# Kernel optimization log

Measured on AMD Instinct MI355X. Metric: run time of the kernel, lower is better.

## Reference

```python
import jax, jax.numpy as jnp
import numpy as np

GAMMA = 1.0 - 2.0 ** (-5)   # 0.96875, as in the module
NUM_GROUPS = 8
NUM_HEADS = 8
EPS = 1e-5


def setup_inputs() -> dict:
    key = jax.random.key(0)
    ks = jax.random.split(key, 8)
    M, S, Hd = 128, 512, 512  # num_segments, bonds per segment, hidden_size
    N = M * S
    return {
        "message": jax.random.normal(ks[0], (N, Hd), jnp.float32),
        "Wq": jax.random.normal(ks[1], (Hd, Hd), jnp.float32) / np.sqrt(Hd).astype(np.float32),
        "Wk": jax.random.normal(ks[2], (Hd, Hd), jnp.float32) / np.sqrt(Hd).astype(np.float32),
        "Wv": jax.random.normal(ks[3], (Hd, Hd), jnp.float32) / np.sqrt(Hd).astype(np.float32),
        "Wo": jax.random.normal(ks[4], (Hd, Hd), jnp.float32) / np.sqrt(Hd).astype(np.float32),
        "bo": jax.random.normal(ks[5], (Hd,), jnp.float32) * 0.01,
        "gn_w": jnp.ones((Hd,), jnp.float32),
        "gn_b": jnp.zeros((Hd,), jnp.float32),
        "num_segs": M,
        "seg_len": S,
    }


def _forward(message, Wq, Wk, Wv, Wo, bo, gn_w, gn_b, M, S):
    Hd = message.shape[1]
    H = NUM_HEADS
    d = Hd // H
    scale = jnp.float32(d ** (-0.5))
    gamma = jnp.float32(GAMMA)

    x = message.reshape(M, S, Hd)                       # equal contiguous segments
    q = (x @ Wq.T).reshape(M, S, H, d)
    k = (x @ Wk.T).reshape(M, S, H, d)
    v = (x @ Wv.T).reshape(M, S, H, d)

    # per-segment K^T V outer-product state contribution: [M, H, d, d]
    A = jnp.einsum('mshd,mshe->mhde', k, v)
    decay = gamma ** S  # gamma ** b_size for equal segments

    def step(r, a):
        # r = K_i^T V_i + gamma^{b_size} * r_prev  (state AFTER segment i, as in source)
        r_new = a + decay * r
        return r_new, r_new

    _, r_all = jax.lax.scan(step, jnp.zeros((H, d, d), x.dtype), A)  # [M, H, d, d]

    # intra-segment retention: (Q K^T) * scale @ V
    scores = jnp.einsum('mshd,mthd->mhst', q, k) * scale
    intra = jnp.einsum('mhst,mthd->mshd', scores, v)
    # cross/recurrent term: (Q @ r_i) * gamma^{i+1}  (note: NOT scaled by scale_factor)
    cross = jnp.einsum('mshd,mhde->mshe', q, r_all)
    g = (gamma ** jnp.arange(1, M + 1, dtype=jnp.float32))[:, None, None, None]
    h = jax.nn.relu(intra + cross * g)                  # activation; dropout p=0

    out = h.reshape(M, S, Hd) @ Wo.T + bo               # W_b_o
    res = x + out                                       # residual (dropout p=0)

    # GroupNorm(8, hidden): per segment (batch N=1), groups over hidden channels,
    # stats pooled over (hidden/8 group channels x S bonds)
    gsh = res.reshape(M, S, NUM_GROUPS, Hd // NUM_GROUPS)
    mean = gsh.mean(axis=(1, 3), keepdims=True)
    var = gsh.var(axis=(1, 3), keepdims=True)
    normed = ((gsh - mean) * jax.lax.rsqrt(var + EPS)).reshape(M, S, Hd)
    normed = normed * gn_w + gn_b

    flat = normed.reshape(M * S, Hd)
    # cached_zero_vector is prepended once before the first segment
    return jnp.concatenate([jnp.zeros((1, Hd), flat.dtype), flat], axis=0)


def reference(message, Wq, Wk, Wv, Wo, bo, gn_w, gn_b, num_segs, seg_len):
    return _forward(message, Wq, Wk, Wv, Wo, bo, gn_w, gn_b, num_segs, seg_len)
```

## Files before the change

kernel.cpp:

```cpp
#include <hip/hip_runtime.h>
#include <math.h>

#define M_SEG 128
#define S_SEG 512
#define HD 512
#define NHEAD 8
#define DHEAD 64
#define NROWS (M_SEG * S_SEG)
#define QKVLD 1536
#define GAMMA_F 0.96875f
#define SCALE_F 0.125f

typedef unsigned short u16;
typedef float f32x4 __attribute__((ext_vector_type(4)));
typedef __bf16 bf16x8 __attribute__((ext_vector_type(8)));
typedef unsigned short ushort8 __attribute__((ext_vector_type(8)));
typedef unsigned short ushort4v __attribute__((ext_vector_type(4)));

__device__ __forceinline__ u16 f2bf(float f) {
    union { float f; unsigned u; } x; x.f = f;
    unsigned r = x.u + 0x7FFFu + ((x.u >> 16) & 1u);
    return (u16)(r >> 16);
}
__device__ __forceinline__ float bf2f(u16 v) {
    union { unsigned u; float f; } x; x.u = ((unsigned)v) << 16;
    return x.f;
}

__device__ __forceinline__ void gload16(const u16* g, u16* l) {
    __builtin_amdgcn_global_load_lds(
        (const __attribute__((address_space(1))) void*)g,
        (__attribute__((address_space(3))) void*)l, 16, 0, 0);
}

__global__ __launch_bounds__(256) void convert_bf16(const float* __restrict__ in,
                                                    u16* __restrict__ outp, int n8)
{
    int idx = blockIdx.x * 256 + threadIdx.x;
    if (idx >= n8) return;
    const float4 a = *reinterpret_cast<const float4*>(&in[(size_t)idx * 8]);
    const float4 b = *reinterpret_cast<const float4*>(&in[(size_t)idx * 8 + 4]);
    ushort8 o;
    o[0] = f2bf(a.x); o[1] = f2bf(a.y); o[2] = f2bf(a.z); o[3] = f2bf(a.w);
    o[4] = f2bf(b.x); o[5] = f2bf(b.y); o[6] = f2bf(b.z); o[7] = f2bf(b.w);
    *reinterpret_cast<ushort8*>(&outp[(size_t)idx * 8]) = o;
}

__global__ __launch_bounds__(256) void convert_weights(const float* __restrict__ w0,
                                                       const float* __restrict__ w1,
                                                       const float* __restrict__ w2,
                                                       const float* __restrict__ w3,
                                                       u16* __restrict__ outp)
{
    const int which = blockIdx.y;
    const float* src = which == 0 ? w0 : which == 1 ? w1 : which == 2 ? w2 : w3;
    u16* dst = outp + (size_t)which * 262144;
    int idx = blockIdx.x * 256 + threadIdx.x;
    const float4 a = *reinterpret_cast<const float4*>(&src[(size_t)idx * 8]);
    const float4 b = *reinterpret_cast<const float4*>(&src[(size_t)idx * 8 + 4]);
    ushort8 o;
    o[0] = f2bf(a.x); o[1] = f2bf(a.y); o[2] = f2bf(a.z); o[3] = f2bf(a.w);
    o[4] = f2bf(b.x); o[5] = f2bf(b.y); o[6] = f2bf(b.z); o[7] = f2bf(b.w);
    *reinterpret_cast<ushort8*>(&dst[(size_t)idx * 8]) = o;
}

template<int EPI>
__global__ __launch_bounds__(512, 1) void gemm8p(const u16* __restrict__ A, int lda,
                                                 const u16* __restrict__ B,
                                                 u16* __restrict__ Cv, int ldc, int ntile,
                                                 const u16* __restrict__ Xb,
                                                 const float* __restrict__ bias)
{
    __shared__ __align__(16) u16 sm[49152];
    const int t    = threadIdx.x;
    const int lane = t & 63;
    const int w    = t >> 6;
    const int wrow = w >> 2;
    const int wcol = w & 3;

    const int nwg  = gridDim.x;
    const int cpx  = nwg >> 3;
    const int bid  = blockIdx.x;
    const int sbid = (bid & 7) * cpx + (bid >> 3);
    const int mt = sbid / ntile, nt = sbid % ntile;
    const int rowBase = mt * 256, colBase = nt * 256;

    const int srow = t >> 2;
    const int sks  = (t & 3) ^ ((srow >> 1) & 3);
    const size_t gA0 = (size_t)(rowBase +       srow) * lda + sks * 8;
    const size_t gA1 = (size_t)(rowBase + 128 + srow) * lda + sks * 8;
    const size_t gB0 = (size_t)(colBase +       srow) * HD  + sks * 8;
    const size_t gB1 = (size_t)(colBase + 128 + srow) * HD  + sks * 8;

    f32x4 acc[8][4];
#pragma unroll
    for (int i = 0; i < 8; ++i)
#pragma unroll
        for (int j = 0; j < 4; ++j)
            acc[i][j] = (f32x4){0.f, 0.f, 0.f, 0.f};

#define STAGE_A(kt, buf)                                                     \
    do {                                                                     \
        gload16(&A[gA0 + (kt) * 32], &sm[(buf) * 16384 + t * 8]);            \
        gload16(&A[gA1 + (kt) * 32], &sm[(buf) * 16384 + 4096 + t * 8]);     \
    } while (0)
#define STAGE_B(kt, buf)                                                     \
    do {                                                                     \
        gload16(&B[gB0 + (kt) * 32], &sm[(buf) * 16384 + 8192 + t * 8]);     \
        gload16(&B[gB1 + (kt) * 32], &sm[(buf) * 16384 + 12288 + t * 8]);    \
    } while (0)

    STAGE_A(0, 0); STAGE_B(0, 0);
    STAGE_A(1, 1); STAGE_B(1, 1);

    const int frow = lane & 15;
    const int fkc  = lane >> 4;

#pragma unroll 1
    for (int kt = 0; kt < 16; ++kt) {
        const int buf = kt % 3;
        const int nbuf = (kt + 2) % 3;

        if (kt < 15) asm volatile("s_waitcnt vmcnt(4)" ::: "memory");
        else         asm volatile("s_waitcnt vmcnt(0)" ::: "memory");
        __builtin_amdgcn_s_barrier();
        __builtin_amdgcn_sched_barrier(0);

        if (kt < 14) STAGE_A(kt + 2, nbuf);
        const u16* Ab = &sm[buf * 16384];
        const u16* Bb = &sm[buf * 16384 + 8192];
        bf16x8 af[4], bfv[4];
#pragma unroll
        for (int mf = 0; mf < 4; ++mf) {
            const int r = wrow * 128 + mf * 16 + frow;
            af[mf] = *reinterpret_cast<const bf16x8*>(&Ab[r * 32 + ((fkc ^ ((r >> 1) & 3)) << 3)]);
        }
#pragma unroll
        for (int nn = 0; nn < 4; ++nn) {
            const int r = wcol * 64 + nn * 16 + frow;
            bfv[nn] = *reinterpret_cast<const bf16x8*>(&Bb[r * 32 + ((fkc ^ ((r >> 1) & 3)) << 3)]);
        }
        __builtin_amdgcn_s_setprio(1);
#pragma unroll
        for (int mf = 0; mf < 4; ++mf)
#pragma unroll
            for (int nn = 0; nn < 4; ++nn)
                acc[mf][nn] = __builtin_amdgcn_mfma_f32_16x16x32_bf16(af[mf], bfv[nn], acc[mf][nn], 0, 0, 0);
        __builtin_amdgcn_s_setprio(0);

        if (kt < 14) STAGE_B(kt + 2, nbuf);
#pragma unroll
        for (int mf = 0; mf < 4; ++mf) {
            const int r = wrow * 128 + 64 + mf * 16 + frow;
            af[mf] = *reinterpret_cast<const bf16x8*>(&Ab[r * 32 + ((fkc ^ ((r >> 1) & 3)) << 3)]);
        }
        __builtin_amdgcn_s_setprio(1);
#pragma unroll
        for (int mf = 0; mf < 4; ++mf)
#pragma unroll
            for (int nn = 0; nn < 4; ++nn)
                acc[4 + mf][nn] = __builtin_amdgcn_mfma_f32_16x16x32_bf16(af[mf], bfv[nn], acc[4 + mf][nn], 0, 0, 0);
        __builtin_amdgcn_s_setprio(0);
    }
#undef STAGE_A
#undef STAGE_B

    const int orow = (lane >> 4) * 4;
    if (EPI == 0) {
        u16* ldsC = sm;
#pragma unroll
        for (int hp = 0; hp < 2; ++hp) {
            __syncthreads();
            if (wrow == hp) {
#pragma unroll
                for (int mm = 0; mm < 8; ++mm)
#pragma unroll
                    for (int nn = 0; nn < 4; ++nn) {
                        const int row0 = mm * 16 + orow;
                        const int col  = wcol * 64 + nn * 16 + frow;
#pragma unroll
                        for (int r = 0; r < 4; ++r)
                            ldsC[(row0 + r) * 256 + col] = f2bf(acc[mm][nn][r]);
                    }
            }
            __syncthreads();
#pragma unroll
            for (int p = 0; p < 8; ++p) {
                const int lin = p * 512 + t;
                const int row = lin >> 5, c8 = lin & 31;
                *reinterpret_cast<ushort8*>(
                    &Cv[(size_t)(rowBase + hp * 128 + row) * ldc + colBase + c8 * 8]) =
                    *reinterpret_cast<const ushort8*>(&ldsC[row * 256 + c8 * 8]);
            }
        }
    } else {
        float* ldsF = (float*)sm;
#pragma unroll
        for (int q = 0; q < 4; ++q) {
            __syncthreads();
            if (wrow == (q >> 1)) {
#pragma unroll
                for (int mm = 0; mm < 4; ++mm) {
                    const int macc = (q & 1) * 4 + mm;
#pragma unroll
                    for (int nn = 0; nn < 4; ++nn) {
                        const int row0 = mm * 16 + orow;
                        const int col  = wcol * 64 + nn * 16 + frow;
#pragma unroll
                        for (int r = 0; r < 4; ++r)
                            ldsF[(row0 + r) * 256 + col] = acc[macc][nn][r];
                    }
                }
            }
            __syncthreads();
#pragma unroll
            for (int p = 0; p < 8; ++p) {
                const int lin = p * 512 + t;
                const int row = lin >> 6, c4 = lin & 63;
                const int grow = rowBase + q * 64 + row;
                float4 a = *reinterpret_cast<const float4*>(&ldsF[row * 256 + c4 * 4]);
                ushort4v x4 = *reinterpret_cast<const ushort4v*>(
                    &Xb[(size_t)grow * HD + colBase + c4 * 4]);
                float4 b = *reinterpret_cast<const float4*>(&bias[colBase + c4 * 4]);
                ushort4v o;
                o[0] = f2bf(a.x + bf2f(x4[0]) + b.x);
                o[1] = f2bf(a.y + bf2f(x4[1]) + b.y);
                o[2] = f2bf(a.z + bf2f(x4[2]) + b.z);
                o[3] = f2bf(a.w + bf2f(x4[3]) + b.w);
                *reinterpret_cast<ushort4v*>(
                    &Cv[(size_t)grow * ldc + colBase + c4 * 4]) = o;
            }
        }
    }
}

__global__ __launch_bounds__(64) void kv_outer(const u16* __restrict__ qkv,
                                               float* __restrict__ Abuf)
{
    __shared__ __align__(16) float Ks[32][64];
    __shared__ __align__(16) float Vs[32][64];
    const int t  = threadIdx.x;
    const int hh = blockIdx.x;
    const int m  = blockIdx.y;
    const int d0 = (t >> 3) * 8;
    const int e0 = (t & 7) * 8;
    float acc[8][8] = {};

    for (int s0 = 0; s0 < S_SEG; s0 += 32) {
#pragma unroll
        for (int i = 0; i < 4; ++i) {
            const int slot = i * 64 + t;
            const int s  = slot >> 3;
            const int c8 = slot & 7;
            size_t g = (size_t)(m * S_SEG + s0 + s) * QKVLD + hh * DHEAD + c8 * 8;
            bf16x8 k8 = *reinterpret_cast<const bf16x8*>(&qkv[g + 512]);
            bf16x8 v8 = *reinterpret_cast<const bf16x8*>(&qkv[g + 1024]);
            float kf[8], vf[8];
#pragma unroll
            for (int j = 0; j < 8; ++j) { kf[j] = (float)k8[j]; vf[j] = (float)v8[j]; }
            *reinterpret_cast<float4*>(&Ks[s][c8 * 8])     = make_float4(kf[0], kf[1], kf[2], kf[3]);
            *reinterpret_cast<float4*>(&Ks[s][c8 * 8 + 4]) = make_float4(kf[4], kf[5], kf[6], kf[7]);
            *reinterpret_cast<float4*>(&Vs[s][c8 * 8])     = make_float4(vf[0], vf[1], vf[2], vf[3]);
            *reinterpret_cast<float4*>(&Vs[s][c8 * 8 + 4]) = make_float4(vf[4], vf[5], vf[6], vf[7]);
        }
        __syncthreads();
#pragma unroll
        for (int s = 0; s < 32; ++s) {
            float4 ka = *reinterpret_cast<const float4*>(&Ks[s][d0]);
            float4 kb = *reinterpret_cast<const float4*>(&Ks[s][d0 + 4]);
            float4 va = *reinterpret_cast<const float4*>(&Vs[s][e0]);
            float4 vb = *reinterpret_cast<const float4*>(&Vs[s][e0 + 4]);
            float kv[8] = {ka.x, ka.y, ka.z, ka.w, kb.x, kb.y, kb.z, kb.w};
            float vv[8] = {va.x, va.y, va.z, va.w, vb.x, vb.y, vb.z, vb.w};
#pragma unroll
            for (int i = 0; i < 8; ++i)
#pragma unroll
                for (int j = 0; j < 8; ++j)
                    acc[i][j] = fmaf(kv[i], vv[j], acc[i][j]);
        }
        __syncthreads();
    }

#pragma unroll
    for (int i = 0; i < 8; ++i) {
        size_t base = ((size_t)(m * NHEAD + hh) * DHEAD + d0 + i) * DHEAD + e0;
        *reinterpret_cast<float4*>(&Abuf[base])     = make_float4(acc[i][0], acc[i][1], acc[i][2], acc[i][3]);
        *reinterpret_cast<float4*>(&Abuf[base + 4]) = make_float4(acc[i][4], acc[i][5], acc[i][6], acc[i][7]);
    }
}

__global__ __launch_bounds__(256) void scan_kernel(const float* __restrict__ Abuf,
                                                   float* __restrict__ Bc)
{
    const int tid = blockIdx.x * 256 + threadIdx.x;
    const float decay = powf(GAMMA_F, (float)S_SEG);
    float r = 0.0f;
    float g = 1.0f;
    for (int m = 0; m < M_SEG; ++m) {
        float a = Abuf[(size_t)m * 32768 + tid];
        r = fmaf(decay, r, a);
        g *= GAMMA_F;
        Bc[(size_t)m * 32768 + tid] = fmaf(g, r, SCALE_F * a);
    }
}

__global__ __launch_bounds__(256) void h_mfma(u16* __restrict__ qkv,
                                              const float* __restrict__ Bc)
{
    __shared__ __align__(16) u16 BT[64 * 72];
    const int t    = threadIdx.x;
    const int lane = t & 63;
    const int w    = t >> 6;
    const int m    = blockIdx.y;
    const int sBase = blockIdx.x * 256 + w * 64;
    const int frow = lane & 15;
    const int fkc  = lane >> 4;

    for (int hh = 0; hh < NHEAD; ++hh) {
#pragma unroll
        for (int i = 0; i < 4; ++i) {
            int idx = t + i * 256;
            int d = idx >> 4, e4 = idx & 15;
            float4 v = *reinterpret_cast<const float4*>(
                &Bc[((size_t)(m * NHEAD + hh) * DHEAD + d) * DHEAD + e4 * 4]);
            BT[(e4 * 4 + 0) * 72 + d] = f2bf(v.x);
            BT[(e4 * 4 + 1) * 72 + d] = f2bf(v.y);
            BT[(e4 * 4 + 2) * 72 + d] = f2bf(v.z);
            BT[(e4 * 4 + 3) * 72 + d] = f2bf(v.w);
        }
        __syncthreads();

        f32x4 acc[4][4];
#pragma unroll
        for (int i = 0; i < 4; ++i)
#pragma unroll
            for (int j = 0; j < 4; ++j)
                acc[i][j] = (f32x4){0.f, 0.f, 0.f, 0.f};

#pragma unroll
        for (int ks = 0; ks < 2; ++ks) {
            bf16x8 af[4], bfr[4];
#pragma unroll
            for (int mm = 0; mm < 4; ++mm) {
                const int grow = m * S_SEG + sBase + mm * 16 + frow;
                af[mm] = *reinterpret_cast<const bf16x8*>(
                    &qkv[(size_t)grow * QKVLD + hh * DHEAD + ks * 32 + fkc * 8]);
                const int e = mm * 16 + frow;
                bfr[mm] = *reinterpret_cast<const bf16x8*>(&BT[e * 72 + ks * 32 + fkc * 8]);
            }
#pragma unroll
            for (int mm = 0; mm < 4; ++mm)
#pragma unroll
                for (int nn = 0; nn < 4; ++nn)
                    acc[mm][nn] = __builtin_amdgcn_mfma_f32_16x16x32_bf16(af[mm], bfr[nn], acc[mm][nn], 0, 0, 0);
        }

        const int orow = (lane >> 4) * 4;
#pragma unroll
        for (int mm = 0; mm < 4; ++mm)
#pragma unroll
            for (int nn = 0; nn < 4; ++nn) {
                const int col  = hh * DHEAD + nn * 16 + frow;
                const int row0 = m * S_SEG + sBase + mm * 16 + orow;
#pragma unroll
                for (int r = 0; r < 4; ++r)
                    qkv[(size_t)(row0 + r) * QKVLD + col] = f2bf(fmaxf(acc[mm][nn][r], 0.f));
            }
        __syncthreads();
    }
}

__global__ __launch_bounds__(256) void groupnorm_bf16(const u16* __restrict__ res,
                                                      float* __restrict__ out,
                                                      const float* __restrict__ gn_w,
                                                      const float* __restrict__ gn_b)
{
    const int g = blockIdx.x;
    const int m = blockIdx.y;
    const int t = threadIdx.x;
    const u16* base = res + (size_t)(m * S_SEG) * QKVLD + g * DHEAD;

    float sum = 0.0f, sq = 0.0f;
    for (int idx = t; idx < 4096; idx += 256) {
        int s = idx >> 3, c8 = idx & 7;
        ushort8 v = *reinterpret_cast<const ushort8*>(&base[(size_t)s * QKVLD + c8 * 8]);
#pragma unroll
        for (int j = 0; j < 8; ++j) {
            float f = bf2f(v[j]);
            sum += f; sq += f * f;
        }
    }
    __shared__ float rs[256], rq[256];
    rs[t] = sum; rq[t] = sq;
    __syncthreads();
    for (int off = 128; off > 0; off >>= 1) {
        if (t < off) { rs[t] += rs[t + off]; rq[t] += rq[t + off]; }
        __syncthreads();
    }
    __shared__ float smean, sinv;
    if (t == 0) {
        float mean = rs[0] * (1.0f / 32768.0f);
        float var  = rq[0] * (1.0f / 32768.0f) - mean * mean;
        smean = mean;
        sinv  = rsqrtf(var + 1e-5f);
    }
    __syncthreads();
    const float mean = smean, inv = sinv;

    for (int idx = t; idx < 4096; idx += 256) {
        int s = idx >> 3, c8 = idx & 7;
        ushort8 v = *reinterpret_cast<const ushort8*>(&base[(size_t)s * QKVLD + c8 * 8]);
        float o[8];
#pragma unroll
        for (int j = 0; j < 8; ++j) {
            float wj = gn_w[g * DHEAD + c8 * 8 + j];
            float bj = gn_b[g * DHEAD + c8 * 8 + j];
            o[j] = (bf2f(v[j]) - mean) * inv * wj + bj;
        }
        float* dst = &out[(size_t)(1 + m * S_SEG + s) * HD + g * DHEAD + c8 * 8];
        *reinterpret_cast<float4*>(dst)     = make_float4(o[0], o[1], o[2], o[3]);
        *reinterpret_cast<float4*>(dst + 4) = make_float4(o[4], o[5], o[6], o[7]);
    }
}

__global__ void zero_row(float* __restrict__ out)
{
    int i = blockIdx.x * 256 + threadIdx.x;
    if (i < HD) out[i] = 0.0f;
}

extern "C" void kernel_launch(void* const* d_in, const int* in_sizes, int n_in,
                              void* d_out, int out_size, void* d_ws, size_t ws_size,
                              hipStream_t stream)
{
    const float* msg = (const float*)d_in[0];
    const float* Wq  = (const float*)d_in[1];
    const float* Wk  = (const float*)d_in[2];
    const float* Wv  = (const float*)d_in[3];
    const float* Wo  = (const float*)d_in[4];
    const float* bo  = (const float*)d_in[5];
    const float* gnw = (const float*)d_in[6];
    const float* gnb = (const float*)d_in[7];
    float* out = (float*)d_out;

    u16*   msgb = (u16*)out;
    float* Abuf = out + 16777216;
    float* Bc   = out + 16777216 + 4194304;

    u16* Wb  = (u16*)d_ws;
    u16* qkv = Wb + 4 * 262144;
    u16* resB = qkv + 512;

    convert_weights<<<dim3(128, 4), 256, 0, stream>>>(Wq, Wk, Wv, Wo, Wb);
    convert_bf16<<<16384, 256, 0, stream>>>(msg, msgb, 4194304);

    gemm8p<0><<<1536, 512, 0, stream>>>(msgb, HD, Wb, qkv, QKVLD, 6, nullptr, nullptr);

    kv_outer<<<dim3(NHEAD, M_SEG), 64, 0, stream>>>(qkv, Abuf);
    scan_kernel<<<128, 256, 0, stream>>>(Abuf, Bc);
    h_mfma<<<dim3(2, M_SEG), 256, 0, stream>>>(qkv, Bc);

    gemm8p<1><<<512, 512, 0, stream>>>(qkv, QKVLD, Wb + 3 * 262144, resB, QKVLD, 2, msgb, bo);

    zero_row<<<2, 256, 0, stream>>>(out);
    groupnorm_bf16<<<dim3(8, M_SEG), 256, 0, stream>>>(resB, out, gnw, gnb);
}
```

Before: 418.3 us.

## Fuse cross-term matmul with output projection and use MFMA for KV outer products

```diff
diff --git a/kernel.cpp b/kernel.cpp
--- a/kernel.cpp
+++ b/kernel.cpp
@@ -26,6 +26,7 @@
     union { unsigned u; float f; } x; x.u = ((unsigned)v) << 16;
     return x.f;
 }
+__device__ __forceinline__ int swzn(int n) { return (n & 3) ^ ((n >> 2) & 3); }
 
 __device__ __forceinline__ void gload16(const u16* g, u16* l) {
     __builtin_amdgcn_global_load_lds(
@@ -64,12 +65,9 @@
     *reinterpret_cast<ushort8*>(&dst[(size_t)idx * 8]) = o;
 }
 
-template<int EPI>
 __global__ __launch_bounds__(512, 1) void gemm8p(const u16* __restrict__ A, int lda,
                                                  const u16* __restrict__ B,
-                                                 u16* __restrict__ Cv, int ldc, int ntile,
-                                                 const u16* __restrict__ Xb,
-                                                 const float* __restrict__ bias)
+                                                 u16* __restrict__ Cv, int ldc, int ntile)
 {
     __shared__ __align__(16) u16 sm[49152];
     const int t    = threadIdx.x;
@@ -166,127 +164,117 @@
 #undef STAGE_B
 
     const int orow = (lane >> 4) * 4;
-    if (EPI == 0) {
-        u16* ldsC = sm;
-#pragma unroll
-        for (int hp = 0; hp < 2; ++hp) {
-            __syncthreads();
-            if (wrow == hp) {
-#pragma unroll
-                for (int mm = 0; mm < 8; ++mm)
-#pragma unroll
-                    for (int nn = 0; nn < 4; ++nn) {
-                        const int row0 = mm * 16 + orow;
-                        const int col  = wcol * 64 + nn * 16 + frow;
-#pragma unroll
-                        for (int r = 0; r < 4; ++r)
-                            ldsC[(row0 + r) * 256 + col] = f2bf(acc[mm][nn][r]);
-                    }
-            }
-            __syncthreads();
-#pragma unroll
-            for (int p = 0; p < 8; ++p) {
-                const int lin = p * 512 + t;
-                const int row = lin >> 5, c8 = lin & 31;
-                *reinterpret_cast<ushort8*>(
-                    &Cv[(size_t)(rowBase + hp * 128 + row) * ldc + colBase + c8 * 8]) =
-                    *reinterpret_cast<const ushort8*>(&ldsC[row * 256 + c8 * 8]);
-            }
-        }
-    } else {
-        float* ldsF = (float*)sm;
-#pragma unroll
-        for (int q = 0; q < 4; ++q) {
-            __syncthreads();
-            if (wrow == (q >> 1)) {
-#pragma unroll
-                for (int mm = 0; mm < 4; ++mm) {
-                    const int macc = (q & 1) * 4 + mm;
-#pragma unroll
-                    for (int nn = 0; nn < 4; ++nn) {
-                        const int row0 = mm * 16 + orow;
-                        const int col  = wcol * 64 + nn * 16 + frow;
-#pragma unroll
-                        for (int r = 0; r < 4; ++r)
-                            ldsF[(row0 + r) * 256 + col] = acc[macc][nn][r];
-                    }
+    u16* ldsC = sm;
+#pragma unroll
+    for (int hp = 0; hp < 2; ++hp) {
+        __syncthreads();
+        if (wrow == hp) {
+#pragma unroll
+            for (int mm = 0; mm < 8; ++mm)
+#pragma unroll
+                for (int nn = 0; nn < 4; ++nn) {
+                    const int row0 = mm * 16 + orow;
+                    const int col  = wcol * 64 + nn * 16 + frow;
+#pragma unroll
+                    for (int r = 0; r < 4; ++r)
+                        ldsC[(row0 + r) * 256 + col] = f2bf(acc[mm][nn][r]);
                 }
-            }
-            __syncthreads();
-#pragma unroll
-            for (int p = 0; p < 8; ++p) {
-                const int lin = p * 512 + t;
-                const int row = lin >> 6, c4 = lin & 63;
-                const int grow = rowBase + q * 64 + row;
-                float4 a = *reinterpret_cast<const float4*>(&ldsF[row * 256 + c4 * 4]);
-                ushort4v x4 = *reinterpret_cast<const ushort4v*>(
-                    &Xb[(size_t)grow * HD + colBase + c4 * 4]);
-                float4 b = *reinterpret_cast<const float4*>(&bias[colBase + c4 * 4]);
-                ushort4v o;
-                o[0] = f2bf(a.x + bf2f(x4[0]) + b.x);
-                o[1] = f2bf(a.y + bf2f(x4[1]) + b.y);
-                o[2] = f2bf(a.z + bf2f(x4[2]) + b.z);
-                o[3] = f2bf(a.w + bf2f(x4[3]) + b.w);
-                *reinterpret_cast<ushort4v*>(
-                    &Cv[(size_t)grow * ldc + colBase + c4 * 4]) = o;
-            }
-        }
-    }
-}
-
-__global__ __launch_bounds__(64) void kv_outer(const u16* __restrict__ qkv,
-                                               float* __restrict__ Abuf)
-{
-    __shared__ __align__(16) float Ks[32][64];
-    __shared__ __align__(16) float Vs[32][64];
-    const int t  = threadIdx.x;
-    const int hh = blockIdx.x;
-    const int m  = blockIdx.y;
-    const int d0 = (t >> 3) * 8;
-    const int e0 = (t & 7) * 8;
-    float acc[8][8] = {};
-
-    for (int s0 = 0; s0 < S_SEG; s0 += 32) {
-#pragma unroll
-        for (int i = 0; i < 4; ++i) {
-            const int slot = i * 64 + t;
-            const int s  = slot >> 3;
-            const int c8 = slot & 7;
-            size_t g = (size_t)(m * S_SEG + s0 + s) * QKVLD + hh * DHEAD + c8 * 8;
-            bf16x8 k8 = *reinterpret_cast<const bf16x8*>(&qkv[g + 512]);
-            bf16x8 v8 = *reinterpret_cast<const bf16x8*>(&qkv[g + 1024]);
-            float kf[8], vf[8];
-#pragma unroll
-            for (int j = 0; j < 8; ++j) { kf[j] = (float)k8[j]; vf[j] = (float)v8[j]; }
-            *reinterpret_cast<float4*>(&Ks[s][c8 * 8])     = make_float4(kf[0], kf[1], kf[2], kf[3]);
-            *reinterpret_cast<float4*>(&Ks[s][c8 * 8 + 4]) = make_float4(kf[4], kf[5], kf[6], kf[7]);
-            *reinterpret_cast<float4*>(&Vs[s][c8 * 8])     = make_float4(vf[0], vf[1], vf[2], vf[3]);
-            *reinterpret_cast<float4*>(&Vs[s][c8 * 8 + 4]) = make_float4(vf[4], vf[5], vf[6], vf[7]);
-        }
-        __syncthreads();
-#pragma unroll
-        for (int s = 0; s < 32; ++s) {
-            float4 ka = *reinterpret_cast<const float4*>(&Ks[s][d0]);
-            float4 kb = *reinterpret_cast<const float4*>(&Ks[s][d0 + 4]);
-            float4 va = *reinterpret_cast<const float4*>(&Vs[s][e0]);
-            float4 vb = *reinterpret_cast<const float4*>(&Vs[s][e0 + 4]);
-            float kv[8] = {ka.x, ka.y, ka.z, ka.w, kb.x, kb.y, kb.z, kb.w};
-            float vv[8] = {va.x, va.y, va.z, va.w, vb.x, vb.y, vb.z, vb.w};
-#pragma unroll
-            for (int i = 0; i < 8; ++i)
-#pragma unroll
-                for (int j = 0; j < 8; ++j)
-                    acc[i][j] = fmaf(kv[i], vv[j], acc[i][j]);
-        }
-        __syncthreads();
-    }
-
-#pragma unroll
-    for (int i = 0; i < 8; ++i) {
-        size_t base = ((size_t)(m * NHEAD + hh) * DHEAD + d0 + i) * DHEAD + e0;
-        *reinterpret_cast<float4*>(&Abuf[base])     = make_float4(acc[i][0], acc[i][1], acc[i][2], acc[i][3]);
-        *reinterpret_cast<float4*>(&Abuf[base + 4]) = make_float4(acc[i][4], acc[i][5], acc[i][6], acc[i][7]);
-    }
+        }
+        __syncthreads();
+#pragma unroll
+        for (int p = 0; p < 8; ++p) {
+            const int lin = p * 512 + t;
+            const int row = lin >> 5, c8 = lin & 31;
+            *reinterpret_cast<ushort8*>(
+                &Cv[(size_t)(rowBase + hp * 128 + row) * ldc + colBase + c8 * 8]) =
+                *reinterpret_cast<const ushort8*>(&ldsC[row * 256 + c8 * 8]);
+        }
+    }
+}
+
+__global__ __launch_bounds__(256) void kv_outer_mfma(const u16* __restrict__ qkv,
+                                                     float* __restrict__ Abuf)
+{
+    __shared__ __align__(16) u16 kT[2048];
+    __shared__ __align__(16) u16 vT[2048];
+    const int t    = threadIdx.x;
+    const int lane = t & 63;
+    const int w    = t >> 6;
+    const int hh   = blockIdx.x;
+    const int m    = blockIdx.y;
+    const int sl   = t & 31;
+    const int dg   = (t >> 5) * 8;
+    const int frow = lane & 15, fkc = lane >> 4, orow = (lane >> 4) * 4;
+    const size_t gbase = (size_t)(m * S_SEG) * QKVLD + 512 + hh * DHEAD + dg;
+
+    f32x4 acc[4];
+#pragma unroll
+    for (int i = 0; i < 4; ++i) acc[i] = (f32x4){0.f, 0.f, 0.f, 0.f};
+
+    ushort8 ka, va, kb, vb;
+
+#define LOADC(c, K8, V8)                                                      \
+    do {                                                                      \
+        size_t g_ = gbase + (size_t)((c) * 32 + sl) * QKVLD;                  \
+        K8 = *reinterpret_cast<const ushort8*>(&qkv[g_]);                     \
+        V8 = *reinterpret_cast<const ushort8*>(&qkv[g_ + 512]);               \
+    } while (0)
+#define WRTC(K8, V8)                                                          \
+    do {                                                                      \
+        _Pragma("unroll")                                                     \
+        for (int j = 0; j < 8; ++j) {                                         \
+            const int d_ = dg + j;                                            \
+            const int a_ = d_ * 32 + ((((sl >> 3) ^ ((d_ >> 1) & 3))) << 3) + (sl & 7); \
+            kT[a_] = K8[j];                                                   \
+            vT[a_] = V8[j];                                                   \
+        }                                                                     \
+    } while (0)
+#define CMPC()                                                                \
+    do {                                                                      \
+        bf16x8 kf[4], vf;                                                     \
+        _Pragma("unroll")                                                     \
+        for (int mf = 0; mf < 4; ++mf) {                                      \
+            const int d_ = mf * 16 + frow;                                    \
+            kf[mf] = *reinterpret_cast<const bf16x8*>(                        \
+                &kT[d_ * 32 + ((fkc ^ ((d_ >> 1) & 3)) << 3)]);               \
+        }                                                                     \
+        const int e_ = w * 16 + frow;                                         \
+        vf = *reinterpret_cast<const bf16x8*>(                                \
+            &vT[e_ * 32 + ((fkc ^ ((e_ >> 1) & 3)) << 3)]);                   \
+        _Pragma("unroll")                                                     \
+        for (int mf = 0; mf < 4; ++mf)                                        \
+            acc[mf] = __builtin_amdgcn_mfma_f32_16x16x32_bf16(kf[mf], vf, acc[mf], 0, 0, 0); \
+    } while (0)
+
+    LOADC(0, ka, va);
+#pragma unroll 1
+    for (int cc = 0; cc < 16; cc += 2) {
+        WRTC(ka, va);
+        LOADC(cc + 1, kb, vb);
+        asm volatile("s_waitcnt lgkmcnt(0)" ::: "memory");
+        __builtin_amdgcn_s_barrier();
+        __builtin_amdgcn_sched_barrier(0);
+        CMPC();
+        __builtin_amdgcn_s_barrier();
+
+        WRTC(kb, vb);
+        if (cc + 2 < 16) LOADC(cc + 2, ka, va);
+        asm volatile("s_waitcnt lgkmcnt(0)" ::: "memory");
+        __builtin_amdgcn_s_barrier();
+        __builtin_amdgcn_sched_barrier(0);
+        CMPC();
+        __builtin_amdgcn_s_barrier();
+    }
+#undef LOADC
+#undef WRTC
+#undef CMPC
+
+    const size_t hb = (size_t)(m * NHEAD + hh) * DHEAD * DHEAD;
+#pragma unroll
+    for (int mf = 0; mf < 4; ++mf)
+#pragma unroll
+        for (int r = 0; r < 4; ++r)
+            Abuf[hb + (size_t)(mf * 16 + orow + r) * DHEAD + w * 16 + frow] = acc[mf][r];
 }
 
 __global__ __launch_bounds__(256) void scan_kernel(const float* __restrict__ Abuf,
@@ -304,69 +292,158 @@
     }
 }
 
-__global__ __launch_bounds__(256) void h_mfma(u16* __restrict__ qkv,
-                                              const float* __restrict__ Bc)
-{
-    __shared__ __align__(16) u16 BT[64 * 72];
+__global__ __launch_bounds__(512, 1) void fuse_ho(const u16* __restrict__ qkv,
+                                                  const float* __restrict__ Bc,
+                                                  const u16* __restrict__ WoB,
+                                                  const u16* __restrict__ msgb,
+                                                  const float* __restrict__ bias,
+                                                  u16* __restrict__ resB)
+{
+    __shared__ __align__(16) u16 smem[81920];
+    u16* hL  = smem;
+    u16* shU = smem + 65536;
     const int t    = threadIdx.x;
     const int lane = t & 63;
     const int w    = t >> 6;
-    const int m    = blockIdx.y;
-    const int sBase = blockIdx.x * 256 + w * 64;
-    const int frow = lane & 15;
-    const int fkc  = lane >> 4;
+    const int frow = lane & 15, fkc = lane >> 4, orow = (lane >> 4) * 4;
+    const int rowBase = blockIdx.x * 128;
+    const int m = rowBase >> 9;
 
     for (int hh = 0; hh < NHEAD; ++hh) {
-#pragma unroll
-        for (int i = 0; i < 4; ++i) {
-            int idx = t + i * 256;
-            int d = idx >> 4, e4 = idx & 15;
+        __syncthreads();
+#pragma unroll
+        for (int i = 0; i < 2; ++i) {
+            const int idx = t + i * 512;
+            const int d = idx >> 4, e4 = idx & 15;
             float4 v = *reinterpret_cast<const float4*>(
                 &Bc[((size_t)(m * NHEAD + hh) * DHEAD + d) * DHEAD + e4 * 4]);
-            BT[(e4 * 4 + 0) * 72 + d] = f2bf(v.x);
-            BT[(e4 * 4 + 1) * 72 + d] = f2bf(v.y);
-            BT[(e4 * 4 + 2) * 72 + d] = f2bf(v.z);
-            BT[(e4 * 4 + 3) * 72 + d] = f2bf(v.w);
-        }
-        __syncthreads();
-
-        f32x4 acc[4][4];
-#pragma unroll
-        for (int i = 0; i < 4; ++i)
-#pragma unroll
-            for (int j = 0; j < 4; ++j)
-                acc[i][j] = (f32x4){0.f, 0.f, 0.f, 0.f};
-
-#pragma unroll
-        for (int ks = 0; ks < 2; ++ks) {
-            bf16x8 af[4], bfr[4];
-#pragma unroll
-            for (int mm = 0; mm < 4; ++mm) {
-                const int grow = m * S_SEG + sBase + mm * 16 + frow;
-                af[mm] = *reinterpret_cast<const bf16x8*>(
-                    &qkv[(size_t)grow * QKVLD + hh * DHEAD + ks * 32 + fkc * 8]);
-                const int e = mm * 16 + frow;
-                bfr[mm] = *reinterpret_cast<const bf16x8*>(&BT[e * 72 + ks * 32 + fkc * 8]);
+            shU[(e4 * 4 + 0) * 72 + d] = f2bf(v.x);
+            shU[(e4 * 4 + 1) * 72 + d] = f2bf(v.y);
+            shU[(e4 * 4 + 2) * 72 + d] = f2bf(v.z);
+            shU[(e4 * 4 + 3) * 72 + d] = f2bf(v.w);
+        }
+        __syncthreads();
+
+        f32x4 a1[4];
+#pragma unroll
+        for (int i = 0; i < 4; ++i) a1[i] = (f32x4){0.f, 0.f, 0.f, 0.f};
+        bf16x8 qf[2];
+#pragma unroll
+        for (int ks = 0; ks < 2; ++ks)
+            qf[ks] = *reinterpret_cast<const bf16x8*>(
+                &qkv[(size_t)(rowBase + w * 16 + frow) * QKVLD + hh * DHEAD + ks * 32 + fkc * 8]);
+#pragma unroll
+        for (int ks = 0; ks < 2; ++ks)
+#pragma unroll
+            for (int nn = 0; nn < 4; ++nn) {
+                bf16x8 bfr = *reinterpret_cast<const bf16x8*>(
+                    &shU[(nn * 16 + frow) * 72 + ks * 32 + fkc * 8]);
+                a1[nn] = __builtin_amdgcn_mfma_f32_16x16x32_bf16(qf[ks], bfr, a1[nn], 0, 0, 0);
             }
 #pragma unroll
-            for (int mm = 0; mm < 4; ++mm)
-#pragma unroll
-                for (int nn = 0; nn < 4; ++nn)
-                    acc[mm][nn] = __builtin_amdgcn_mfma_f32_16x16x32_bf16(af[mm], bfr[nn], acc[mm][nn], 0, 0, 0);
-        }
-
-        const int orow = (lane >> 4) * 4;
-#pragma unroll
-        for (int mm = 0; mm < 4; ++mm)
-#pragma unroll
-            for (int nn = 0; nn < 4; ++nn) {
-                const int col  = hh * DHEAD + nn * 16 + frow;
-                const int row0 = m * S_SEG + sBase + mm * 16 + orow;
-#pragma unroll
-                for (int r = 0; r < 4; ++r)
-                    qkv[(size_t)(row0 + r) * QKVLD + col] = f2bf(fmaxf(acc[mm][nn][r], 0.f));
+        for (int nn = 0; nn < 4; ++nn)
+#pragma unroll
+            for (int r = 0; r < 4; ++r) {
+                const int row = w * 16 + orow + r;
+                const int col = hh * DHEAD + nn * 16 + frow;
+                hL[row * 512 + (col ^ ((row & 7) << 3))] = f2bf(fmaxf(a1[nn][r], 0.f));
             }
-        __syncthreads();
+    }
+    __syncthreads();
+
+    f32x4 acc[8][4];
+#pragma unroll
+    for (int i = 0; i < 8; ++i)
+#pragma unroll
+        for (int j = 0; j < 4; ++j)
+            acc[i][j] = (f32x4){0.f, 0.f, 0.f, 0.f};
+
+    ushort8 ra[4], rb[4];
+#define LOADW(kt, rr)                                                         \
+    do {                                                                      \
+        _Pragma("unroll")                                                     \
+        for (int c = 0; c < 4; ++c)                                           \
+            rr[c] = *reinterpret_cast<const ushort8*>(                        \
+                &WoB[(size_t)t * 512 + (kt) * 32 + c * 8]);                   \
+    } while (0)
+#define WRTW(rr)                                                              \
+    do {                                                                      \
+        _Pragma("unroll")                                                     \
+        for (int c = 0; c < 4; ++c)                                           \
+            *reinterpret_cast<ushort8*>(&shU[t * 32 + ((c ^ swzn(t)) << 3)]) = rr[c]; \
+    } while (0)
+#define CMPW(kt)                                                              \
+    do {                                                                      \
+        bf16x8 bf[4];                                                         \
+        _Pragma("unroll")                                                     \
+        for (int nn = 0; nn < 4; ++nn) {                                      \
+            const int n2 = w * 64 + nn * 16 + frow;                           \
+            bf[nn] = *reinterpret_cast<const bf16x8*>(                        \
+                &shU[n2 * 32 + ((fkc ^ swzn(n2)) << 3)]);                     \
+        }                                                                     \
+        _Pragma("unroll")                                                     \
+        for (int mm = 0; mm < 8; ++mm) {                                      \
+            const int row = mm * 16 + frow;                                   \
+            bf16x8 af = *reinterpret_cast<const bf16x8*>(                     \
+                &hL[row * 512 + (((kt) * 32 + fkc * 8) ^ ((row & 7) << 3))]); \
+            _Pragma("unroll")                                                 \
+            for (int nn = 0; nn < 4; ++nn)                                    \
+                acc[mm][nn] = __builtin_amdgcn_mfma_f32_16x16x32_bf16(af, bf[nn], acc[mm][nn], 0, 0, 0); \
+        }                                                                     \
+    } while (0)
+
+    LOADW(0, ra);
+#pragma unroll 1
+    for (int kt = 0; kt < 16; kt += 2) {
+        WRTW(ra);
+        LOADW(kt + 1, rb);
+        asm volatile("s_waitcnt lgkmcnt(0)" ::: "memory");
+        __builtin_amdgcn_s_barrier();
+        __builtin_amdgcn_sched_barrier(0);
+        __builtin_amdgcn_s_setprio(1);
+        CMPW(kt);
+        __builtin_amdgcn_s_setprio(0);
+        __builtin_amdgcn_s_barrier();
+
+        WRTW(rb);
+        if (kt + 2 < 16) LOADW(kt + 2, ra);
+        asm volatile("s_waitcnt lgkmcnt(0)" ::: "memory");
+        __builtin_amdgcn_s_barrier();
+        __builtin_amdgcn_sched_barrier(0);
+        __builtin_amdgcn_s_setprio(1);
+        CMPW(kt + 1);
+        __builtin_amdgcn_s_setprio(0);
+        __builtin_amdgcn_s_barrier();
+    }
+#undef LOADW
+#undef WRTW
+#undef CMPW
+
+    float* ldsF = (float*)shU;
+#pragma unroll 1
+    for (int p = 0; p < 8; ++p) {
+        __syncthreads();
+#pragma unroll
+        for (int nn = 0; nn < 4; ++nn)
+#pragma unroll
+            for (int r = 0; r < 4; ++r)
+                ldsF[(orow + r) * 512 + w * 64 + nn * 16 + frow] = acc[p][nn][r];
+        __syncthreads();
+#pragma unroll
+        for (int i = 0; i < 4; ++i) {
+            const int lin = i * 512 + t;
+            const int row = lin >> 7, c4 = lin & 127;
+            const int grow = rowBase + p * 16 + row;
+            float4 a = *reinterpret_cast<const float4*>(&ldsF[row * 512 + c4 * 4]);
+            ushort4v x = *reinterpret_cast<const ushort4v*>(&msgb[(size_t)grow * HD + c4 * 4]);
+            float4 b = *reinterpret_cast<const float4*>(&bias[c4 * 4]);
+            ushort4v o;
+            o[0] = f2bf(a.x + bf2f(x[0]) + b.x);
+            o[1] = f2bf(a.y + bf2f(x[1]) + b.y);
+            o[2] = f2bf(a.z + bf2f(x[2]) + b.z);
+            o[3] = f2bf(a.w + bf2f(x[3]) + b.w);
+            *reinterpret_cast<ushort4v*>(&resB[(size_t)grow * QKVLD + c4 * 4]) = o;
+        }
     }
 }
 
@@ -447,20 +524,19 @@
     float* Abuf = out + 16777216;
     float* Bc   = out + 16777216 + 4194304;
 
-    u16* Wb  = (u16*)d_ws;
-    u16* qkv = Wb + 4 * 262144;
+    u16* Wb   = (u16*)d_ws;
+    u16* qkv  = Wb + 4 * 262144;
     u16* resB = qkv + 512;
 
     convert_weights<<<dim3(128, 4), 256, 0, stream>>>(Wq, Wk, Wv, Wo, Wb);
     convert_bf16<<<16384, 256, 0, stream>>>(msg, msgb, 4194304);
 
-    gemm8p<0><<<1536, 512, 0, stream>>>(msgb, HD, Wb, qkv, QKVLD, 6, nullptr, nullptr);
-
-    kv_outer<<<dim3(NHEAD, M_SEG), 64, 0, stream>>>(qkv, Abuf);
+    gemm8p<<<1536, 512, 0, stream>>>(msgb, HD, Wb, qkv, QKVLD, 6);
+
+    kv_outer_mfma<<<dim3(NHEAD, M_SEG), 256, 0, stream>>>(qkv, Abuf);
     scan_kernel<<<128, 256, 0, stream>>>(Abuf, Bc);
-    h_mfma<<<dim3(2, M_SEG), 256, 0, stream>>>(qkv, Bc);
-
-    gemm8p<1><<<512, 512, 0, stream>>>(qkv, QKVLD, Wb + 3 * 262144, resB, QKVLD, 2, msgb, bo);
+
+    fuse_ho<<<512, 512, 0, stream>>>(qkv, Bc, Wb + 3 * 262144, msgb, bo, resB);
 
     zero_row<<<2, 256, 0, stream>>>(out);
     groupnorm_bf16<<<dim3(8, M_SEG), 256, 0, stream>>>(resB, out, gnw, gnb);
```

Result: slower. 427.9 us (+2.3%).
